# Performance work log

Measured on AMD Instinct MI355X. Metric: run time of the kernel, lower is better.

Reference implementation:

```python
import jax, jax.numpy as jnp
import numpy as np

V, D, H, F, L, B, T = 32000, 512, 8, 2048, 4, 4, 1024
DK = D // H
S = 0.02  # init scale


def setup_inputs() -> dict:
    key = jax.random.key(0)
    ks = jax.random.split(key, 10)
    inp = {
        'x': jax.random.randint(ks[0], (B, T), 0, V),
        'embed': jax.random.normal(ks[1], (V, D), jnp.float32) * S,
        'Wq': jax.random.normal(ks[2], (L, D, D), jnp.float32) * S,
        'bq': jnp.zeros((L, D), jnp.float32),
        'Wk': jax.random.normal(ks[3], (L, D, D), jnp.float32) * S,
        'bk': jnp.zeros((L, D), jnp.float32),
        'Wv': jax.random.normal(ks[4], (L, D, D), jnp.float32) * S,
        'bv': jnp.zeros((L, D), jnp.float32),
        'Wo': jax.random.normal(ks[5], (L, D, D), jnp.float32) * S,
        'bo': jnp.zeros((L, D), jnp.float32),
        'ln1_s': jnp.ones((L, D), jnp.float32),
        'ln1_b': jnp.zeros((L, D), jnp.float32),
        'W1': jax.random.normal(ks[6], (L, D, F), jnp.float32) * S,
        'b1': jnp.zeros((L, F), jnp.float32),
        'W2': jax.random.normal(ks[7], (L, F, D), jnp.float32) * S,
        'b2': jnp.zeros((L, D), jnp.float32),
        'ln2_s': jnp.ones((L, D), jnp.float32),
        'ln2_b': jnp.zeros((L, D), jnp.float32),
        'lnf_s': jnp.ones((D,), jnp.float32),
        'lnf_b': jnp.zeros((D,), jnp.float32),
        'Wl': jax.random.normal(ks[8], (D, V), jnp.float32) * S,
        'bl': jnp.zeros((V,), jnp.float32),
    }
    return inp


def _layernorm(x, s, b, eps=1e-5):
    m = jnp.mean(x, axis=-1, keepdims=True)
    v = jnp.mean(jnp.square(x - m), axis=-1, keepdims=True)
    return (x - m) * jax.lax.rsqrt(v + eps) * s + b


def _forward(x, embed, Wq, bq, Wk, bk, Wv, bv, Wo, bo, ln1_s, ln1_b,
             W1, b1, W2, b2, ln2_s, ln2_b, lnf_s, lnf_b, Wl, bl):
    Bb, Tt = x.shape
    emb = embed.at[0].set(0.0)  # padding_idx = 0
    h = emb[x]  # [B,T,D]
    # sinusoidal positional encoding
    pos = jnp.arange(Tt, dtype=jnp.float32)[:, None]
    div = jnp.exp(jnp.arange(0, D, 2, dtype=jnp.float32) * (-np.log(10000.0) / D))
    pe = jnp.zeros((Tt, D), jnp.float32)
    pe = pe.at[:, 0::2].set(jnp.sin(pos * div)).at[:, 1::2].set(jnp.cos(pos * div))
    h = h + pe[None]
    # additive causal mask: 0 on/below diag, -inf above
    causal = jnp.triu(jnp.full((Tt, Tt), -jnp.inf, jnp.float32), 1)
    scale = 1.0 / np.sqrt(DK)
    for l in range(L):
        q = (h @ Wq[l] + bq[l]).reshape(Bb, Tt, H, DK)
        k = (h @ Wk[l] + bk[l]).reshape(Bb, Tt, H, DK)
        v = (h @ Wv[l] + bv[l]).reshape(Bb, Tt, H, DK)
        scores = jnp.einsum('bqhd,bkhd->bhqk', q, k) * scale + causal
        attn = jax.nn.softmax(scores, axis=-1)  # dropout=0 -> identity
        o = jnp.einsum('bhqk,bkhd->bqhd', attn, v).reshape(Bb, Tt, D)
        o = o @ Wo[l] + bo[l]
        h = _layernorm(h + o, ln1_s[l], ln1_b[l])
        ff = jax.nn.gelu(h @ W1[l] + b1[l], approximate=False) @ W2[l] + b2[l]
        h = _layernorm(h + ff, ln2_s[l], ln2_b[l])
    h = _layernorm(h, lnf_s, lnf_b)
    return h @ Wl + bl  # [B,T,V] logits


def reference(x, embed, Wq, bq, Wk, bk, Wv, bv, Wo, bo, ln1_s, ln1_b,
              W1, b1, W2, b2, ln2_s, ln2_b, lnf_s, lnf_b, Wl, bl):
    return _forward(x, embed, Wq, bq, Wk, bk, Wv, bv, Wo, bo, ln1_s, ln1_b,
                    W1, b1, W2, b2, ln2_s, ln2_b, lnf_s, lnf_b, Wl, bl)
```

## Files before the change

### kernel.cpp

```cpp
#include <hip/hip_runtime.h>
#include <math.h>

#define Mtot 4096
#define Dd   512
#define Hh   8
#define DKk  64
#define TT   1024
#define Ff   2048
#define Ll   4
#define Vv   32000

typedef __attribute__((ext_vector_type(8))) short bf16x8;
typedef __attribute__((ext_vector_type(4))) float f32x4;
typedef unsigned short u16;

__device__ __forceinline__ u16 f2b(float f) {
    union { float f; unsigned u; } x; x.f = f;
    unsigned r = x.u + 0x7fffu + ((x.u >> 16) & 1u);
    return (u16)(r >> 16);
}

typedef const __attribute__((address_space(1))) unsigned int* gp_t;
typedef __attribute__((address_space(3))) unsigned int* lp_t;
#define GLOAD_LDS16(g, l) __builtin_amdgcn_global_load_lds((gp_t)(const void*)(g), (lp_t)(void*)(l), 16, 0, 0)
#define SBAR  __builtin_amdgcn_s_barrier()
#define SCHED0 __builtin_amdgcn_sched_barrier(0)

#define SWZ(row, c)  ((c) ^ (((row) & 7) << 3))

__global__ __launch_bounds__(256) void prep_kernel(const float* __restrict__ Wq, const float* __restrict__ Wk,
                                                   const float* __restrict__ Wv, const float* __restrict__ Wo,
                                                   const float* __restrict__ W1, const float* __restrict__ W2,
                                                   const float* __restrict__ Wl,
                                                   u16* __restrict__ WqkvT, u16* __restrict__ WoT,
                                                   u16* __restrict__ W1T, u16* __restrict__ W2T,
                                                   u16* __restrict__ WlT,
                                                   const float* __restrict__ bq, const float* __restrict__ bk,
                                                   const float* __restrict__ bv, float* __restrict__ bqkv,
                                                   const int* __restrict__ x, const float* __restrict__ emw,
                                                   float* __restrict__ h, u16* __restrict__ hb) {
    int id = blockIdx.x;
    if (id >= 28312) {
        int idx = (id - 28312) * 256 + threadIdx.x;
        int d  = idx & (Dd - 1);
        int bt = idx >> 9;
        int t  = bt & (TT - 1);
        int tok = x[bt];
        float val = (tok == 0) ? 0.0f : emw[(size_t)tok * Dd + d];
        int de = d & ~1;
        float ang = (float)t * expf((float)de * (-9.210340371976184f / (float)Dd));
        val += (d & 1) ? cosf(ang) : sinf(ang);
        h[idx] = val;
        hb[idx] = f2b(val);
        return;
    }
    if (id >= 28288) {
        int idx = (id - 28288) * 256 + threadIdx.x;
        int l = idx / 1536, j = idx - l * 1536;
        float v = (j < 512) ? bq[l * 512 + j] : (j < 1024) ? bk[l * 512 + j - 512] : bv[l * 512 + j - 1024];
        bqkv[idx] = v;
        return;
    }
    __shared__ float t[32][33];
    const float* src; u16* dst; int K, N, tx, ty;
    if (id < 12288) {
        int l = id / 3072, r = id - l * 3072;
        if (r < 768) {
            int which = r >> 8, t2 = r & 255;
            src = (which == 0 ? Wq : which == 1 ? Wk : Wv) + (size_t)l * 262144;
            dst = WqkvT + (size_t)l * 786432 + (size_t)which * 262144;
            K = 512; N = 512; ty = t2 >> 4; tx = t2 & 15;
        } else if (r < 1024) {
            int t2 = r - 768;
            src = Wo + (size_t)l * 262144; dst = WoT + (size_t)l * 262144;
            K = 512; N = 512; ty = t2 >> 4; tx = t2 & 15;
        } else if (r < 2048) {
            int t2 = r - 1024;
            src = W1 + (size_t)l * 1048576; dst = W1T + (size_t)l * 1048576;
            K = 512; N = 2048; ty = t2 >> 6; tx = t2 & 63;
        } else {
            int t2 = r - 2048;
            src = W2 + (size_t)l * 1048576; dst = W2T + (size_t)l * 1048576;
            K = 2048; N = 512; ty = t2 >> 4; tx = t2 & 15;
        }
    } else {
        int t2 = id - 12288;
        src = Wl; dst = WlT; K = 512; N = 32000;
        ty = t2 / 1000; tx = t2 - ty * 1000;
    }
    int n0 = tx * 32, k0 = ty * 32;
    int tid = threadIdx.x, c = tid & 31, rr = tid >> 5;
    #pragma unroll
    for (int i = 0; i < 4; i++)
        t[rr + i * 8][c] = src[(size_t)(k0 + rr + i * 8) * N + n0 + c];
    __syncthreads();
    #pragma unroll
    for (int i = 0; i < 4; i++)
        dst[(size_t)(n0 + rr + i * 8) * K + k0 + c] = f2b(t[c][rr + i * 8]);
}

template<int ACT, int OUTB, int QKVMODE, int SPLITK>
__global__ __launch_bounds__(256, 2) void mfma_gemm(const u16* __restrict__ A,
                                                    const u16* __restrict__ BT,
                                                    const float* __restrict__ bias,
                                                    float* __restrict__ outF,
                                                    u16* __restrict__ outB,
                                                    u16* __restrict__ vtb,
                                                    int M, int N, int K, int gx, int PS) {
    __shared__ __align__(16) u16 As[2][128 * 64];
    __shared__ __align__(16) u16 Bs[2][128 * 64];
    int tid = threadIdx.x;
    int lane = tid & 63, w = tid >> 6;
    int nwg = gridDim.x, flat = blockIdx.x;
    int wg = (flat & 7) * (nwg >> 3) + (flat >> 3);
    int ks = 0, sub = wg;
    if (SPLITK > 1) {
        int tps = gx * (M >> 7);
        ks = wg / tps; sub = wg - ks * tps;
    }
    int bm = sub / gx, bn = sub - bm * gx;
    int kb = ks * (K / SPLITK);
    int wr = w >> 1, wc = w & 1;
    int fr = lane & 15, fq = lane >> 4;

    int sr = lane >> 3, sc = lane & 7;
    int scol = (sc ^ sr) * 8;
    const u16* Ab = A  + (size_t)(bm * 128 + w * 32 + sr) * K + kb + scol;
    const u16* Bb = BT + (size_t)(bn * 128 + w * 32 + sr) * K + kb + scol;
    u16* lA = &As[0][0] + w * 2048;
    u16* lB = &Bs[0][0] + w * 2048;

    f32x4 acc[4][4] = {};
    int nk = (K / SPLITK) >> 6;

#define STAGE(buf, kt)                                                     \
    {   int ko = (kt) * 64;                                                \
        GLOAD_LDS16(Ab + ko,          lA + (buf) * (128 * 64));            \
        GLOAD_LDS16(Ab + 8 * K + ko,  lA + (buf) * (128 * 64) + 512);      \
        GLOAD_LDS16(Ab + 16 * K + ko, lA + (buf) * (128 * 64) + 1024);     \
        GLOAD_LDS16(Ab + 24 * K + ko, lA + (buf) * (128 * 64) + 1536);     \
        GLOAD_LDS16(Bb + ko,          lB + (buf) * (128 * 64));            \
        GLOAD_LDS16(Bb + 8 * K + ko,  lB + (buf) * (128 * 64) + 512);      \
        GLOAD_LDS16(Bb + 16 * K + ko, lB + (buf) * (128 * 64) + 1024);     \
        GLOAD_LDS16(Bb + 24 * K + ko, lB + (buf) * (128 * 64) + 1536); }

    STAGE(0, 0);
    STAGE(1, 1);

    int cur = 0;
    for (int kt = 0; kt < nk; kt++) {
        if (kt + 1 < nk) { asm volatile("s_waitcnt vmcnt(8)" ::: "memory"); }
        else             { asm volatile("s_waitcnt vmcnt(0)" ::: "memory"); }
        SBAR;
        SCHED0;
        bf16x8 a[4][2], b[4][2];
        #pragma unroll
        for (int m = 0; m < 4; m++) {
            int row = wr * 64 + m * 16 + fr;
            a[m][0] = *(const bf16x8*)&As[cur][row * 64 + ((fq ^ (row & 7)) * 8)];
            a[m][1] = *(const bf16x8*)&As[cur][row * 64 + (((fq + 4) ^ (row & 7)) * 8)];
        }
        #pragma unroll
        for (int n = 0; n < 4; n++) {
            int row = wc * 64 + n * 16 + fr;
            b[n][0] = *(const bf16x8*)&Bs[cur][row * 64 + ((fq ^ (row & 7)) * 8)];
            b[n][1] = *(const bf16x8*)&Bs[cur][row * 64 + (((fq + 4) ^ (row & 7)) * 8)];
        }
        __builtin_amdgcn_s_setprio(1);
        #pragma unroll
        for (int m = 0; m < 4; m++)
            #pragma unroll
            for (int n = 0; n < 4; n++) {
                acc[m][n] = __builtin_amdgcn_mfma_f32_16x16x32_bf16(b[n][0], a[m][0], acc[m][n], 0, 0, 0);
                acc[m][n] = __builtin_amdgcn_mfma_f32_16x16x32_bf16(b[n][1], a[m][1], acc[m][n], 0, 0, 0);
            }
        __builtin_amdgcn_s_setprio(0);
        SCHED0;
        SBAR;
        SCHED0;
        if (kt + 2 < nk) STAGE(cur, kt + 2);
        cur ^= 1;
    }
#undef STAGE

    #pragma unroll
    for (int m = 0; m < 4; m++) {
        int row = bm * 128 + wr * 64 + m * 16 + fr;
        #pragma unroll
        for (int n = 0; n < 4; n++) {
            int col0 = bn * 128 + wc * 64 + n * 16 + fq * 4;
            if (QKVMODE && bn >= 8) {
                int bb = row >> 10, t = row & 1023;
                #pragma unroll
                for (int r = 0; r < 4; r++) {
                    int d = col0 + r - 1024;
                    int hh = d >> 6, dd = d & 63;
                    vtb[(((size_t)bb * Hh + hh) * 64 + dd) * 1024 + t] = f2b(acc[m][n][r] + bias[col0 + r]);
                }
            } else {
                f32x4 v = acc[m][n];
                if (bias && ks == 0) v += *(const f32x4*)&bias[col0];
                if (ACT == 1) {
                    #pragma unroll
                    for (int r = 0; r < 4; r++) v[r] = 0.5f * v[r] * (1.0f + erff(v[r] * 0.7071067811865475f));
                }
                if (OUTB) {
                    union { unsigned long long ull; u16 s[4]; } pk;
                    #pragma unroll
                    for (int r = 0; r < 4; r++) pk.s[r] = f2b(v[r]);
                    *(unsigned long long*)&outB[(size_t)row * N + col0] = pk.ull;
                } else {
                    *(f32x4*)&outF[(size_t)ks * PS + (size_t)row * N + col0] = v;
                }
            }
        }
    }
}

__global__ __launch_bounds__(512, 1) void mfma_gemm256(const u16* __restrict__ A,
                                                       const u16* __restrict__ BT,
                                                       const float* __restrict__ bias,
                                                       float* __restrict__ outF,
                                                       int M, int N, int K, int gy) {
    __shared__ __align__(16) u16 As[2][256 * 64];
    __shared__ __align__(16) u16 Bs[2][256 * 64];
    int tid = threadIdx.x;
    int lane = tid & 63, w = tid >> 6;
    int nwg = gridDim.x, flat = blockIdx.x;
    int wg = (flat & 7) * (nwg >> 3) + (flat >> 3);
    int bm = wg & (gy - 1), bn = wg >> 4;
    int wr = w >> 2, wc = w & 3;
    int fr = lane & 15, fq = lane >> 4;

    int sr8 = lane >> 3, sc = lane & 7;
    int scol = (sc ^ sr8) * 8;
    const u16* Ab = A  + (size_t)(bm * 256 + w * 32 + sr8) * K + scol;
    const u16* Bb = BT + (size_t)(bn * 256 + w * 32 + sr8) * K + scol;

    f32x4 acc[8][4] = {};
    int nk = K >> 6;

#define STAGE256(buf, kt)                                                    \
    {   int ko = (kt) * 64;                                                  \
        GLOAD_LDS16(Ab + ko,          &As[buf][(w * 32 +  0) * 64]);         \
        GLOAD_LDS16(Ab + 8 * K + ko,  &As[buf][(w * 32 +  8) * 64]);         \
        GLOAD_LDS16(Ab + 16 * K + ko, &As[buf][(w * 32 + 16) * 64]);         \
        GLOAD_LDS16(Ab + 24 * K + ko, &As[buf][(w * 32 + 24) * 64]);         \
        GLOAD_LDS16(Bb + ko,          &Bs[buf][(w * 32 +  0) * 64]);         \
        GLOAD_LDS16(Bb + 8 * K + ko,  &Bs[buf][(w * 32 +  8) * 64]);         \
        GLOAD_LDS16(Bb + 16 * K + ko, &Bs[buf][(w * 32 + 16) * 64]);         \
        GLOAD_LDS16(Bb + 24 * K + ko, &Bs[buf][(w * 32 + 24) * 64]); }

    STAGE256(0, 0);
    STAGE256(1, 1);

    int cur = 0;
    for (int kt = 0; kt < nk; kt++) {
        if (kt + 1 < nk) { asm volatile("s_waitcnt vmcnt(8)" ::: "memory"); }
        else             { asm volatile("s_waitcnt vmcnt(0)" ::: "memory"); }
        SBAR;
        SCHED0;
        bf16x8 b[4][2];
        #pragma unroll
        for (int n = 0; n < 4; n++) {
            int row = wc * 64 + n * 16 + fr;
            b[n][0] = *(const bf16x8*)&Bs[cur][row * 64 + ((fq ^ (row & 7)) * 8)];
            b[n][1] = *(const bf16x8*)&Bs[cur][row * 64 + (((fq + 4) ^ (row & 7)) * 8)];
        }
        #pragma unroll
        for (int m = 0; m < 8; m++) {
            int row = wr * 128 + m * 16 + fr;
            bf16x8 a0 = *(const bf16x8*)&As[cur][row * 64 + ((fq ^ (row & 7)) * 8)];
            bf16x8 a1 = *(const bf16x8*)&As[cur][row * 64 + (((fq + 4) ^ (row & 7)) * 8)];
            __builtin_amdgcn_s_setprio(1);
            #pragma unroll
            for (int n = 0; n < 4; n++) {
                acc[m][n] = __builtin_amdgcn_mfma_f32_16x16x32_bf16(b[n][0], a0, acc[m][n], 0, 0, 0);
                acc[m][n] = __builtin_amdgcn_mfma_f32_16x16x32_bf16(b[n][1], a1, acc[m][n], 0, 0, 0);
            }
            __builtin_amdgcn_s_setprio(0);
        }
        SCHED0;
        SBAR;
        SCHED0;
        if (kt + 2 < nk) STAGE256(cur, kt + 2);
        cur ^= 1;
    }
#undef STAGE256

    #pragma unroll
    for (int m = 0; m < 8; m++) {
        int row = bm * 256 + wr * 128 + m * 16 + fr;
        #pragma unroll
        for (int n = 0; n < 4; n++) {
            int col0 = bn * 256 + wc * 64 + n * 16 + fq * 4;
            f32x4 v = acc[m][n] + *(const f32x4*)&bias[col0];
            *(f32x4*)&outF[(size_t)row * N + col0] = v;
        }
    }
}

__global__ __launch_bounds__(256) void attn_mfma(const u16* __restrict__ qkv,
                                                 const u16* __restrict__ vtb,
                                                 u16* __restrict__ ob) {
    int qt = (int)gridDim.x - 1 - (int)blockIdx.x;
    int hh = blockIdx.y, b = blockIdx.z;
    __shared__ __align__(16) u16 Qs[64 * 64];
    __shared__ __align__(16) u16 Ks[64 * 64];
    __shared__ __align__(16) u16 Vs[64 * 64];
    __shared__ __align__(16) u16 Ps[4][16 * 64];
    int tid = threadIdx.x;
    int lane = tid & 63, w = tid >> 6;
    int fr = lane & 15, fq = lane >> 4;
    int q0 = qt * 64;
    int sr = tid >> 2, sc0 = (tid & 3) * 16;

    bf16x8 rk0, rk1, rv0, rv1;
    bf16x8 sk0, sk1, sv0, sv1;

    auto load_a = [&](int kt) {
        const u16* srcK = qkv + ((size_t)(b * TT + kt * 64 + sr)) * 1536 + 512 + hh * 64 + sc0;
        rk0 = *(const bf16x8*)srcK; rk1 = *(const bf16x8*)(srcK + 8);
        const u16* srcV = vtb + (((size_t)(b * Hh + hh)) * 64 + sr) * 1024 + kt * 64 + sc0;
        rv0 = *(const bf16x8*)srcV; rv1 = *(const bf16x8*)(srcV + 8);
    };
    auto load_b = [&](int kt) {
        const u16* srcK = qkv + ((size_t)(b * TT + kt * 64 + sr)) * 1536 + 512 + hh * 64 + sc0;
        sk0 = *(const bf16x8*)srcK; sk1 = *(const bf16x8*)(srcK + 8);
        const u16* srcV = vtb + (((size_t)(b * Hh + hh)) * 64 + sr) * 1024 + kt * 64 + sc0;
        sv0 = *(const bf16x8*)srcV; sv1 = *(const bf16x8*)(srcV + 8);
    };
    auto store_a = [&]() {
        *(bf16x8*)&Ks[sr * 64 + SWZ(sr, sc0)]     = rk0;
        *(bf16x8*)&Ks[sr * 64 + SWZ(sr, sc0 + 8)] = rk1;
        *(bf16x8*)&Vs[sr * 64 + SWZ(sr, sc0)]     = rv0;
        *(bf16x8*)&Vs[sr * 64 + SWZ(sr, sc0 + 8)] = rv1;
    };
    auto store_b = [&]() {
        *(bf16x8*)&Ks[sr * 64 + SWZ(sr, sc0)]     = sk0;
        *(bf16x8*)&Ks[sr * 64 + SWZ(sr, sc0 + 8)] = sk1;
        *(bf16x8*)&Vs[sr * 64 + SWZ(sr, sc0)]     = sv0;
        *(bf16x8*)&Vs[sr * 64 + SWZ(sr, sc0 + 8)] = sv1;
    };

    load_a(0);
    {
        const u16* src = qkv + ((size_t)(b * TT + q0 + sr)) * 1536 + hh * 64 + sc0;
        bf16x8 v0 = *(const bf16x8*)src;
        bf16x8 v1 = *(const bf16x8*)(src + 8);
        *(bf16x8*)&Qs[sr * 64 + SWZ(sr, sc0)]     = v0;
        *(bf16x8*)&Qs[sr * 64 + SWZ(sr, sc0 + 8)] = v1;
    }
    __syncthreads();
    bf16x8 aq0 = *(const bf16x8*)&Qs[(w * 16 + fr) * 64 + SWZ(w * 16 + fr, fq * 8)];
    bf16x8 aq1 = *(const bf16x8*)&Qs[(w * 16 + fr) * 64 + SWZ(w * 16 + fr, 32 + fq * 8)];

    f32x4 oa[4] = {};
    float mreg[4], lreg[4];
    #pragma unroll
    for (int i = 0; i < 4; i++) { mreg[i] = -1e30f; lreg[i] = 0.0f; }

    auto compute_tile = [&](int kt) {
        f32x4 sa[4] = {};
        __builtin_amdgcn_s_setprio(1);
        #pragma unroll
        for (int nt = 0; nt < 4; nt++) {
            int krow = nt * 16 + fr;
            bf16x8 b0 = *(const bf16x8*)&Ks[krow * 64 + SWZ(krow, fq * 8)];
            bf16x8 b1 = *(const bf16x8*)&Ks[krow * 64 + SWZ(krow, 32 + fq * 8)];
            sa[nt] = __builtin_amdgcn_mfma_f32_16x16x32_bf16(aq0, b0, sa[nt], 0, 0, 0);
            sa[nt] = __builtin_amdgcn_mfma_f32_16x16x32_bf16(aq1, b1, sa[nt], 0, 0, 0);
        }
        __builtin_amdgcn_s_setprio(0);

        float p[4][4];
        int qg = w * 16 + fq * 4;
        bool diag = (kt == qt);
        #pragma unroll
        for (int nt = 0; nt < 4; nt++)
            #pragma unroll
            for (int i = 0; i < 4; i++) {
                float s = sa[nt][i] * 0.125f;
                if (diag && (nt * 16 + fr > qg + i)) s = -1e30f;
                p[nt][i] = s;
            }

        float mnew[4], fscale[4];
        #pragma unroll
        for (int i = 0; i < 4; i++) {
            float v = fmaxf(fmaxf(p[0][i], p[1][i]), fmaxf(p[2][i], p[3][i]));
            v = fmaxf(v, __shfl_xor(v, 1));
            v = fmaxf(v, __shfl_xor(v, 2));
            v = fmaxf(v, __shfl_xor(v, 4));
            v = fmaxf(v, __shfl_xor(v, 8));
            mnew[i] = fmaxf(mreg[i], v);
            fscale[i] = __expf(mreg[i] - mnew[i]);
            mreg[i] = mnew[i];
        }
        #pragma unroll
        for (int i = 0; i < 4; i++) {
            float sum = 0.f;
            #pragma unroll
            for (int nt = 0; nt < 4; nt++) {
                float e = __expf(p[nt][i] - mnew[i]);
                p[nt][i] = e;
                sum += e;
            }
            sum += __shfl_xor(sum, 1);
            sum += __shfl_xor(sum, 2);
            sum += __shfl_xor(sum, 4);
            sum += __shfl_xor(sum, 8);
            lreg[i] = lreg[i] * fscale[i] + sum;
        }
        #pragma unroll
        for (int nn = 0; nn < 4; nn++)
            #pragma unroll
            for (int i = 0; i < 4; i++)
                oa[nn][i] *= fscale[i];

        u16* ps = &Ps[w][0];
        #pragma unroll
        for (int nt = 0; nt < 4; nt++)
            #pragma unroll
            for (int i = 0; i < 4; i++) {
                int row = fq * 4 + i, col = nt * 16 + fr;
                ps[row * 64 + SWZ(row, col)] = f2b(p[nt][i]);
            }
        bf16x8 pa0 = *(const bf16x8*)&ps[fr * 64 + SWZ(fr, fq * 8)];
        bf16x8 pa1 = *(const bf16x8*)&ps[fr * 64 + SWZ(fr, 32 + fq * 8)];
        __builtin_amdgcn_s_setprio(1);
        #pragma unroll
        for (int nn = 0; nn < 4; nn++) {
            int drow = nn * 16 + fr;
            bf16x8 vb0 = *(const bf16x8*)&Vs[drow * 64 + SWZ(drow, fq * 8)];
            bf16x8 vb1 = *(const bf16x8*)&Vs[drow * 64 + SWZ(drow, 32 + fq * 8)];
            oa[nn] = __builtin_amdgcn_mfma_f32_16x16x32_bf16(pa0, vb0, oa[nn], 0, 0, 0);
            oa[nn] = __builtin_amdgcn_mfma_f32_16x16x32_bf16(pa1, vb1, oa[nn], 0, 0, 0);
        }
        __builtin_amdgcn_s_setprio(0);
    };

    int kt = 0;
    for (;;) {
        SCHED0; SBAR;
        store_a();
        if (kt + 1 <= qt) load_b(kt + 1);
        asm volatile("s_waitcnt lgkmcnt(0)" ::: "memory");
        SBAR; SCHED0;
        compute_tile(kt);
        if (++kt > qt) break;

        SCHED0; SBAR;
        store_b();
        if (kt + 1 <= qt) load_a(kt + 1);
        asm volatile("s_waitcnt lgkmcnt(0)" ::: "memory");
        SBAR; SCHED0;
        compute_tile(kt);
        if (++kt > qt) break;
    }

    #pragma unroll
    for (int i = 0; i < 4; i++) {
        float inv = 1.0f / lreg[i];
        size_t row = (size_t)(b * TT + q0 + w * 16 + fq * 4 + i) * Dd + hh * 64;
        #pragma unroll
        for (int nn = 0; nn < 4; nn++)
            ob[row + nn * 16 + fr] = f2b(oa[nn][i] * inv);
    }
}

__global__ __launch_bounds__(256) void ln_kernel(float* __restrict__ h,
                                                 const float* __restrict__ pp, int np,
                                                 const float* __restrict__ gs,
                                                 const float* __restrict__ gb,
                                                 const float* __restrict__ gs2,
                                                 const float* __restrict__ gb2,
                                                 u16* __restrict__ hb) {
    int w = threadIdx.x >> 6, lane = threadIdx.x & 63;
    int row = (blockIdx.x << 2) + w;
    size_t base = (size_t)row * Dd + lane * 8;
    const size_t PART = (size_t)Mtot * Dd;
    f32x4 v0 = *(const f32x4*)&h[base];
    f32x4 v1 = *(const f32x4*)&h[base + 4];
    for (int p = 0; p < np; p++) {
        const float* d = pp + (size_t)p * PART;
        v0 += *(const f32x4*)&d[base];
        v1 += *(const f32x4*)&d[base + 4];
    }
    float s = v0[0] + v0[1] + v0[2] + v0[3] + v1[0] + v1[1] + v1[2] + v1[3];
    #pragma unroll
    for (int st = 1; st < 64; st <<= 1) s += __shfl_xor(s, st);
    float m = s * (1.0f / Dd);
    float q = 0.f;
    #pragma unroll
    for (int j = 0; j < 4; j++) { float a = v0[j] - m, b = v1[j] - m; q += a * a + b * b; }
    #pragma unroll
    for (int st = 1; st < 64; st <<= 1) q += __shfl_xor(q, st);
    float r = rsqrtf(q * (1.0f / Dd) + 1e-5f);
    f32x4 g0 = *(const f32x4*)&gs[lane * 8],     g1 = *(const f32x4*)&gs[lane * 8 + 4];
    f32x4 c0 = *(const f32x4*)&gb[lane * 8],     c1 = *(const f32x4*)&gb[lane * 8 + 4];
    f32x4 y0, y1;
    #pragma unroll
    for (int j = 0; j < 4; j++) {
        y0[j] = (v0[j] - m) * r * g0[j] + c0[j];
        y1[j] = (v1[j] - m) * r * g1[j] + c1[j];
    }
    if (gs2) {
        float s2 = y0[0] + y0[1] + y0[2] + y0[3] + y1[0] + y1[1] + y1[2] + y1[3];
        #pragma unroll
        for (int st = 1; st < 64; st <<= 1) s2 += __shfl_xor(s2, st);
        float m2 = s2 * (1.0f / Dd);
        float q2 = 0.f;
        #pragma unroll
        for (int j = 0; j < 4; j++) { float a = y0[j] - m2, b = y1[j] - m2; q2 += a * a + b * b; }
        #pragma unroll
        for (int st = 1; st < 64; st <<= 1) q2 += __shfl_xor(q2, st);
        float r2 = rsqrtf(q2 * (1.0f / Dd) + 1e-5f);
        f32x4 h0 = *(const f32x4*)&gs2[lane * 8], h1 = *(const f32x4*)&gs2[lane * 8 + 4];
        f32x4 d0 = *(const f32x4*)&gb2[lane * 8], d1 = *(const f32x4*)&gb2[lane * 8 + 4];
        #pragma unroll
        for (int j = 0; j < 4; j++) {
            y0[j] = (y0[j] - m2) * r2 * h0[j] + d0[j];
            y1[j] = (y1[j] - m2) * r2 * h1[j] + d1[j];
        }
    }
    bf16x8 yb;
    #pragma unroll
    for (int j = 0; j < 4; j++) {
        yb[j]     = (short)f2b(y0[j]);
        yb[j + 4] = (short)f2b(y1[j]);
    }
    *(f32x4*)&h[base]     = y0;
    *(f32x4*)&h[base + 4] = y1;
    *(bf16x8*)&hb[base]   = yb;
}

extern "C" void kernel_launch(void* const* d_in, const int* in_sizes, int n_in,
                              void* d_out, int out_size, void* d_ws, size_t ws_size,
                              hipStream_t stream) {
    const int*   x     = (const int*)  d_in[0];
    const float* embed = (const float*)d_in[1];
    const float* Wq    = (const float*)d_in[2];
    const float* bq    = (const float*)d_in[3];
    const float* Wk    = (const float*)d_in[4];
    const float* bk    = (const float*)d_in[5];
    const float* Wv    = (const float*)d_in[6];
    const float* bv    = (const float*)d_in[7];
    const float* Wo    = (const float*)d_in[8];
    const float* bo    = (const float*)d_in[9];
    const float* ln1_s = (const float*)d_in[10];
    const float* ln1_b = (const float*)d_in[11];
    const float* W1    = (const float*)d_in[12];
    const float* b1    = (const float*)d_in[13];
    const float* W2    = (const float*)d_in[14];
    const float* b2    = (const float*)d_in[15];
    const float* ln2_s = (const float*)d_in[16];
    const float* ln2_b = (const float*)d_in[17];
    const float* lnf_s = (const float*)d_in[18];
    const float* lnf_b = (const float*)d_in[19];
    const float* Wl    = (const float*)d_in[20];
    const float* bl    = (const float*)d_in[21];

    char* wp = (char*)d_ws;
    float* h    = (float*)wp;  wp += (size_t)Mtot * Dd * 4;
    u16*   hb   = (u16*)wp;    wp += (size_t)Mtot * Dd * 2;
    u16*   qkvb = (u16*)wp;    wp += (size_t)Mtot * 1536 * 2;
    u16*   vtb  = (u16*)wp;    wp += (size_t)Mtot * Dd * 2;
    u16*   obb  = (u16*)wp;    wp += (size_t)Mtot * Dd * 2;
    u16*   fbb  = (u16*)wp;    wp += (size_t)Mtot * Ff * 2;
    u16*   WlT  = (u16*)wp;    wp += (size_t)Vv * Dd * 2;
    float* bqkv = (float*)wp;  wp += (size_t)Ll * 1536 * 4;

    char* op = (char*)d_out;
    u16* WqkvT = (u16*)op;  op += (size_t)Ll * 1536 * Dd * 2;
    u16* WoT   = (u16*)op;  op += (size_t)Ll * Dd * Dd * 2;
    u16* W1T   = (u16*)op;  op += (size_t)Ll * Ff * Dd * 2;
    u16* W2T   = (u16*)op;  op += (size_t)Ll * Dd * Ff * 2;
    float* pbx = (float*)op; op += (size_t)4 * Mtot * Dd * 4;

    prep_kernel<<<36504, 256, 0, stream>>>(Wq, Wk, Wv, Wo, W1, W2, Wl,
                                           WqkvT, WoT, W1T, W2T, WlT,
                                           bq, bk, bv, bqkv, x, embed, h, hb);

    const int PS = Mtot * Dd;

    for (int l = 0; l < Ll; l++) {
        mfma_gemm<0, 1, 1, 1><<<(1536 / 128) * (Mtot / 128), 256, 0, stream>>>(
            hb, WqkvT + (size_t)l * 1536 * Dd, bqkv + l * 1536, nullptr, qkvb, vtb,
            Mtot, 1536, Dd, 1536 / 128, 0);
        attn_mfma<<<dim3(TT / 64, Hh, 4), 256, 0, stream>>>(qkvb, vtb, obb);
        mfma_gemm<0, 0, 0, 2><<<2 * (Dd / 128) * (Mtot / 128), 256, 0, stream>>>(
            obb, WoT + (size_t)l * Dd * Dd, bo + l * Dd, pbx, nullptr, nullptr,
            Mtot, Dd, Dd, Dd / 128, PS);
        ln_kernel<<<Mtot / 4, 256, 0, stream>>>(h, pbx, 2, ln1_s + l * Dd, ln1_b + l * Dd,
                                                nullptr, nullptr, hb);
        mfma_gemm<1, 1, 0, 1><<<(Ff / 128) * (Mtot / 128), 256, 0, stream>>>(
            hb, W1T + (size_t)l * Ff * Dd, b1 + l * Ff, nullptr, fbb, nullptr,
            Mtot, Ff, Dd, Ff / 128, 0);
        mfma_gemm<0, 0, 0, 4><<<4 * (Dd / 128) * (Mtot / 128), 256, 0, stream>>>(
            fbb, W2T + (size_t)l * Dd * Ff, b2 + l * Dd, pbx, nullptr, nullptr,
            Mtot, Dd, Ff, Dd / 128, PS);
        ln_kernel<<<Mtot / 4, 256, 0, stream>>>(h, pbx, 4, ln2_s + l * Dd, ln2_b + l * Dd,
                                                (l == Ll - 1) ? lnf_s : nullptr,
                                                (l == Ll - 1) ? lnf_b : nullptr, hb);
    }

    mfma_gemm256<<<(Vv / 256) * (Mtot / 256), 512, 0, stream>>>(
        hb, WlT, bl, (float*)d_out, Mtot, Vv, Dd, Mtot / 256);
}
```

Baseline: 758.5 us.

## Use 128-row query tiles in attention and halve W2 split-K partials

The attention kernel now runs 512-thread blocks covering 128 query rows, so each loaded K/V tile is shared by eight waves instead of four. The K and V loads are split across thread halves, and the causal mask is computed from global indices on every tile. Separately, the W2 projection GEMM drops from 4-way to 2-way split-K, which halves the partial buffers the following layernorm must read. In exchange the attention grid has half as many blocks, with more causal imbalance and masked work per block, and each W2 GEMM block loops over twice as much K.

Result: slower. 775.6 us (+2.2%).

```diff
diff --git a/kernel.cpp b/kernel.cpp
--- a/kernel.cpp
+++ b/kernel.cpp
@@ -300,56 +300,44 @@
     }
 }
 
-__global__ __launch_bounds__(256) void attn_mfma(const u16* __restrict__ qkv,
+__global__ __launch_bounds__(512) void attn_mfma(const u16* __restrict__ qkv,
                                                  const u16* __restrict__ vtb,
                                                  u16* __restrict__ ob) {
     int qt = (int)gridDim.x - 1 - (int)blockIdx.x;
     int hh = blockIdx.y, b = blockIdx.z;
-    __shared__ __align__(16) u16 Qs[64 * 64];
+    __shared__ __align__(16) u16 Qs[128 * 64];
     __shared__ __align__(16) u16 Ks[64 * 64];
     __shared__ __align__(16) u16 Vs[64 * 64];
-    __shared__ __align__(16) u16 Ps[4][16 * 64];
+    __shared__ __align__(16) u16 Ps[8][16 * 64];
     int tid = threadIdx.x;
     int lane = tid & 63, w = tid >> 6;
     int fr = lane & 15, fq = lane >> 4;
-    int q0 = qt * 64;
-    int sr = tid >> 2, sc0 = (tid & 3) * 16;
-
-    bf16x8 rk0, rk1, rv0, rv1;
-    bf16x8 sk0, sk1, sv0, sv1;
-
-    auto load_a = [&](int kt) {
-        const u16* srcK = qkv + ((size_t)(b * TT + kt * 64 + sr)) * 1536 + 512 + hh * 64 + sc0;
-        rk0 = *(const bf16x8*)srcK; rk1 = *(const bf16x8*)(srcK + 8);
-        const u16* srcV = vtb + (((size_t)(b * Hh + hh)) * 64 + sr) * 1024 + kt * 64 + sc0;
-        rv0 = *(const bf16x8*)srcV; rv1 = *(const bf16x8*)(srcV + 8);
-    };
-    auto load_b = [&](int kt) {
-        const u16* srcK = qkv + ((size_t)(b * TT + kt * 64 + sr)) * 1536 + 512 + hh * 64 + sc0;
-        sk0 = *(const bf16x8*)srcK; sk1 = *(const bf16x8*)(srcK + 8);
-        const u16* srcV = vtb + (((size_t)(b * Hh + hh)) * 64 + sr) * 1024 + kt * 64 + sc0;
-        sv0 = *(const bf16x8*)srcV; sv1 = *(const bf16x8*)(srcV + 8);
-    };
-    auto store_a = [&]() {
-        *(bf16x8*)&Ks[sr * 64 + SWZ(sr, sc0)]     = rk0;
-        *(bf16x8*)&Ks[sr * 64 + SWZ(sr, sc0 + 8)] = rk1;
-        *(bf16x8*)&Vs[sr * 64 + SWZ(sr, sc0)]     = rv0;
-        *(bf16x8*)&Vs[sr * 64 + SWZ(sr, sc0 + 8)] = rv1;
-    };
-    auto store_b = [&]() {
-        *(bf16x8*)&Ks[sr * 64 + SWZ(sr, sc0)]     = sk0;
-        *(bf16x8*)&Ks[sr * 64 + SWZ(sr, sc0 + 8)] = sk1;
-        *(bf16x8*)&Vs[sr * 64 + SWZ(sr, sc0)]     = sv0;
-        *(bf16x8*)&Vs[sr * 64 + SWZ(sr, sc0 + 8)] = sv1;
-    };
-
-    load_a(0);
+    int q0 = qt * 128;
+    int nkt = 2 * qt + 2;
+
+    int kv = tid >> 8;
+    int rr = (tid & 255) >> 2, cc = ((tid & 255) & 3) * 16;
+    const u16* kvbase;
+    size_t kstep;
+    if (kv == 0) { kvbase = qkv + ((size_t)(b * TT + rr)) * 1536 + 512 + hh * 64 + cc; kstep = (size_t)64 * 1536; }
+    else         { kvbase = vtb + (((size_t)(b * Hh + hh)) * 64 + rr) * 1024 + cc;     kstep = 64; }
+    u16* lds0 = (kv ? Vs : Ks) + rr * 64 + SWZ(rr, cc);
+    u16* lds1 = (kv ? Vs : Ks) + rr * 64 + SWZ(rr, cc + 8);
+
+    bf16x8 r0, r1, s0, s1;
+    auto load_cur = [&](int kt) { const u16* p = kvbase + (size_t)kt * kstep; r0 = *(const bf16x8*)p; r1 = *(const bf16x8*)(p + 8); };
+    auto load_nxt = [&](int kt) { const u16* p = kvbase + (size_t)kt * kstep; s0 = *(const bf16x8*)p; s1 = *(const bf16x8*)(p + 8); };
+    auto store_cur = [&]() { *(bf16x8*)lds0 = r0; *(bf16x8*)lds1 = r1; };
+    auto store_nxt = [&]() { *(bf16x8*)lds0 = s0; *(bf16x8*)lds1 = s1; };
+
+    load_cur(0);
     {
-        const u16* src = qkv + ((size_t)(b * TT + q0 + sr)) * 1536 + hh * 64 + sc0;
+        int r = tid >> 2, c0 = (tid & 3) * 16;
+        const u16* src = qkv + ((size_t)(b * TT + q0 + r)) * 1536 + hh * 64 + c0;
         bf16x8 v0 = *(const bf16x8*)src;
         bf16x8 v1 = *(const bf16x8*)(src + 8);
-        *(bf16x8*)&Qs[sr * 64 + SWZ(sr, sc0)]     = v0;
-        *(bf16x8*)&Qs[sr * 64 + SWZ(sr, sc0 + 8)] = v1;
+        *(bf16x8*)&Qs[r * 64 + SWZ(r, c0)]     = v0;
+        *(bf16x8*)&Qs[r * 64 + SWZ(r, c0 + 8)] = v1;
     }
     __syncthreads();
     bf16x8 aq0 = *(const bf16x8*)&Qs[(w * 16 + fr) * 64 + SWZ(w * 16 + fr, fq * 8)];
@@ -374,14 +362,14 @@
         __builtin_amdgcn_s_setprio(0);
 
         float p[4][4];
-        int qg = w * 16 + fq * 4;
-        bool diag = (kt == qt);
+        int qgb = q0 + w * 16 + fq * 4;
+        int kgb = kt * 64 + fr;
         #pragma unroll
         for (int nt = 0; nt < 4; nt++)
             #pragma unroll
             for (int i = 0; i < 4; i++) {
                 float s = sa[nt][i] * 0.125f;
-                if (diag && (nt * 16 + fr > qg + i)) s = -1e30f;
+                if (kgb + nt * 16 > qgb + i) s = -1e30f;
                 p[nt][i] = s;
             }
 
@@ -443,20 +431,20 @@
     int kt = 0;
     for (;;) {
         SCHED0; SBAR;
-        store_a();
-        if (kt + 1 <= qt) load_b(kt + 1);
+        store_cur();
+        if (kt + 1 < nkt) load_nxt(kt + 1);
         asm volatile("s_waitcnt lgkmcnt(0)" ::: "memory");
         SBAR; SCHED0;
         compute_tile(kt);
-        if (++kt > qt) break;
+        if (++kt >= nkt) break;
 
         SCHED0; SBAR;
-        store_b();
-        if (kt + 1 <= qt) load_a(kt + 1);
+        store_nxt();
+        if (kt + 1 < nkt) load_cur(kt + 1);
         asm volatile("s_waitcnt lgkmcnt(0)" ::: "memory");
         SBAR; SCHED0;
         compute_tile(kt);
-        if (++kt > qt) break;
+        if (++kt >= nkt) break;
     }
 
     #pragma unroll
@@ -576,7 +564,7 @@
     u16* WoT   = (u16*)op;  op += (size_t)Ll * Dd * Dd * 2;
     u16* W1T   = (u16*)op;  op += (size_t)Ll * Ff * Dd * 2;
     u16* W2T   = (u16*)op;  op += (size_t)Ll * Dd * Ff * 2;
-    float* pbx = (float*)op; op += (size_t)4 * Mtot * Dd * 4;
+    float* pbx = (float*)op; op += (size_t)2 * Mtot * Dd * 4;
 
     prep_kernel<<<36504, 256, 0, stream>>>(Wq, Wk, Wv, Wo, W1, W2, Wl,
                                            WqkvT, WoT, W1T, W2T, WlT,
@@ -588,7 +576,7 @@
         mfma_gemm<0, 1, 1, 1><<<(1536 / 128) * (Mtot / 128), 256, 0, stream>>>(
             hb, WqkvT + (size_t)l * 1536 * Dd, bqkv + l * 1536, nullptr, qkvb, vtb,
             Mtot, 1536, Dd, 1536 / 128, 0);
-        attn_mfma<<<dim3(TT / 64, Hh, 4), 256, 0, stream>>>(qkvb, vtb, obb);
+        attn_mfma<<<dim3(TT / 128, Hh, 4), 512, 0, stream>>>(qkvb, vtb, obb);
         mfma_gemm<0, 0, 0, 2><<<2 * (Dd / 128) * (Mtot / 128), 256, 0, stream>>>(
             obb, WoT + (size_t)l * Dd * Dd, bo + l * Dd, pbx, nullptr, nullptr,
             Mtot, Dd, Dd, Dd / 128, PS);
@@ -597,10 +585,10 @@
         mfma_gemm<1, 1, 0, 1><<<(Ff / 128) * (Mtot / 128), 256, 0, stream>>>(
             hb, W1T + (size_t)l * Ff * Dd, b1 + l * Ff, nullptr, fbb, nullptr,
             Mtot, Ff, Dd, Ff / 128, 0);
-        mfma_gemm<0, 0, 0, 4><<<4 * (Dd / 128) * (Mtot / 128), 256, 0, stream>>>(
+        mfma_gemm<0, 0, 0, 2><<<2 * (Dd / 128) * (Mtot / 128), 256, 0, stream>>>(
             fbb, W2T + (size_t)l * Dd * Ff, b2 + l * Dd, pbx, nullptr, nullptr,
             Mtot, Dd, Ff, Dd / 128, PS);
-        ln_kernel<<<Mtot / 4, 256, 0, stream>>>(h, pbx, 4, ln2_s + l * Dd, ln2_b + l * Dd,
+        ln_kernel<<<Mtot / 4, 256, 0, stream>>>(h, pbx, 2, ln2_s + l * Dd, ln2_b + l * Dd,
                                                 (l == Ll - 1) ? lnf_s : nullptr,
                                                 (l == Ll - 1) ? lnf_b : nullptr, hb);
     }
```
